# Kernel tuning notes

Hardware: AMD Instinct MI355X
Metric: run time of the kernel (lower is better)

The kernel has to match this reference:

```python
import jax, jax.numpy as jnp
import numpy as np

B, C, D = 4, 2048, 1024
DCONV, DMAMBA, K, DSTATE = 512, 512, 4, 16
FFN = 2560


def setup_inputs() -> dict:
    key = jax.random.key(0)
    ks = jax.random.split(key, 16)
    n = lambda k, shape, s=1.0: jax.random.normal(k, shape, jnp.float32) * s
    inv = lambda f: 1.0 / float(np.sqrt(f))
    return {
        "x": n(ks[0], (B, C, D)),
        "velocity": n(ks[1], (B, C, D), 0.1),
        "v_hat_chunk": n(ks[2], (B, C, D)),
        "delta_W": n(ks[3], (FFN, D), 0.01),
        "pre_norm_w": jnp.ones((D,), jnp.float32),
        "ffn_norm_w": jnp.ones((D,), jnp.float32),
        "conv_in_w": n(ks[4], (D, 2 * DCONV), inv(D)),
        "conv_kernel_w": n(ks[5], (K, 1, DCONV), inv(K)),
        "ssm_in_w": n(ks[6], (D, 2 * DMAMBA), inv(D)),
        "ssm_dt_w": n(ks[7], (D, DMAMBA), inv(D)),
        "ssm_dt_b": jnp.full((DMAMBA,), -4.0, jnp.float32),
        "ssm_A_log": jnp.tile(jnp.log(jnp.arange(1.0, DSTATE + 1, dtype=jnp.float32)), (DMAMBA, 1)),
        "ssm_B_w": n(ks[8], (D, DSTATE), inv(D)),
        "ssm_C_w": n(ks[9], (D, DSTATE), inv(D)),
        "ssm_D": jnp.ones((DMAMBA,), jnp.float32),
        "out_proj_w": n(ks[10], (D, D), inv(D)),
        "log_beta": jnp.array(0.0, jnp.float32),  # sigmoid -> beta=0.5
        "ffn_gate_up_w": n(ks[11], (D, 2 * FFN), inv(D)),
        "ffn_down_w": n(ks[12], (FFN, D), inv(FFN)),
        "ffn_target_w": n(ks[13], (D, FFN), inv(D)),
        "log_gamma": jnp.array(0.0, jnp.float32),
        "log_eta": jnp.array(-4.0, jnp.float32),
    }


def _rms(x, w, eps=1e-6):
    return x * jax.lax.rsqrt(jnp.mean(x * x, axis=-1, keepdims=True) + eps) * w


def _gated_conv(xn, w_in, kernel):
    # proj -> split gate/value, depthwise causal conv on value, silu-gate
    g, v = jnp.split(xn @ w_in, 2, axis=-1)  # (B,C,DCONV) each
    v = jax.lax.conv_general_dilated(
        v, kernel, window_strides=(1,), padding=[(K - 1, 0)],
        dimension_numbers=("NWC", "WIO", "NWC"), feature_group_count=DCONV)
    return jax.nn.silu(g) * v


def _ssm(xn, w_in, w_dt, dt_b, A_log, w_B, w_C, Dp):
    # Mamba-style selective SISO scan
    u, z = jnp.split(xn @ w_in, 2, axis=-1)          # (B,C,DMAMBA)
    dt = jax.nn.softplus(xn @ w_dt + dt_b)            # (B,C,DMAMBA)
    A = -jnp.exp(A_log)                               # (DMAMBA,DSTATE)
    Bs = xn @ w_B                                     # (B,C,DSTATE)
    Cs = xn @ w_C                                     # (B,C,DSTATE)
    dA = jnp.exp(dt[..., None] * A)                   # (B,C,DMAMBA,DSTATE)
    dBu = (dt * u)[..., None] * Bs[:, :, None, :]     # (B,C,DMAMBA,DSTATE)

    def step(h, inputs):
        dA_t, dBu_t, C_t = inputs
        h = dA_t * h + dBu_t                          # (B,DMAMBA,DSTATE)
        return h, jnp.einsum("bds,bs->bd", h, C_t)

    xs = (jnp.moveaxis(dA, 1, 0), jnp.moveaxis(dBu, 1, 0), jnp.moveaxis(Cs, 1, 0))
    _, ys = jax.lax.scan(step, jnp.zeros((B, DMAMBA, DSTATE), xn.dtype), xs)
    y = jnp.moveaxis(ys, 0, 1) + Dp * u               # (B,C,DMAMBA)
    return y * jax.nn.silu(z)


def reference(x, velocity, v_hat_chunk, delta_W, pre_norm_w, ffn_norm_w,
              conv_in_w, conv_kernel_w, ssm_in_w, ssm_dt_w, ssm_dt_b, ssm_A_log,
              ssm_B_w, ssm_C_w, ssm_D, out_proj_w, log_beta, ffn_gate_up_w,
              ffn_down_w, ffn_target_w, log_gamma, log_eta):
    xn = _rms(x, pre_norm_w)
    conv_out = _gated_conv(xn, conv_in_w, conv_kernel_w)
    ssm_out = _ssm(xn, ssm_in_w, ssm_dt_w, ssm_dt_b, ssm_A_log, ssm_B_w, ssm_C_w, ssm_D)
    mixed = jnp.concatenate([conv_out, ssm_out], axis=-1) @ out_proj_w
    # momentum residual
    velocity = jax.nn.sigmoid(log_beta) * velocity + mixed
    x = x + velocity
    # Living SwiGLU
    ffn_in = _rms(x, ffn_norm_w)
    gate, up = jnp.split(ffn_in @ ffn_gate_up_w, 2, axis=-1)
    z = jax.nn.silu(gate) * up                        # (B,C,FFN)
    out = z @ ffn_down_w + z @ delta_W                # fast-weight augmented down proj
    v_hat_proj = v_hat_chunk @ ffn_target_w           # (B,C,FFN)
    update = jnp.einsum("bcf,bcd->fd", v_hat_proj, ffn_in) / x.shape[0]
    new_delta_W = jax.nn.sigmoid(log_gamma) * delta_W + jax.nn.softplus(log_eta) * update
    x = x + out
    return (x, velocity, new_delta_W)
```

## Files before the change

kernel.cpp:

```cpp
#include <hip/hip_runtime.h>
#include <stdint.h>
#include <stddef.h>

#define B_ 4
#define C_ 2048
#define D_ 1024
#define FFN_ 2560
#define ROWS_ 8192

typedef unsigned short u16;
typedef short bf16x8 __attribute__((ext_vector_type(8)));
typedef float f32x4 __attribute__((ext_vector_type(4)));

__device__ __forceinline__ float bf2f(u16 x){ union { unsigned u; float f; } v; v.u = ((unsigned)x)<<16; return v.f; }
__device__ __forceinline__ u16 f2bf(float f){ union { float f; unsigned u; } v; v.f = f; unsigned r = v.u + 0x7fffu + ((v.u>>16)&1u); return (u16)(r>>16); }
__device__ __forceinline__ float sigm_(float x){ return 1.f/(1.f+__expf(-x)); }
__device__ __forceinline__ float silu_(float x){ return x/(1.f+__expf(-x)); }
__device__ __forceinline__ float softplus_(float x){ return (x>15.f)? x : log1pf(__expf(x)); }

__device__ __forceinline__ void async16(u16* lds_base, const u16* g){
  __builtin_amdgcn_global_load_lds((const __attribute__((address_space(1))) unsigned int*)g,
                                   (__attribute__((address_space(3))) unsigned int*)lds_base,
                                   16, 0, 0);
}

#define EPI_INPROJ 0
#define EPI_MOM    1
#define EPI_SWIGLU 2
#define EPI_TRANS  3
#define EPI_ATOMX  4
#define EPI_ATOMD  5

template<int EPI>
__global__ __launch_bounds__(256)
void gemm128(const u16* __restrict__ A, const u16* __restrict__ Bt,
             int M, int N, int K, int ksplit,
             float* __restrict__ f0, float* __restrict__ f1,
             const float* __restrict__ c0, const float* __restrict__ c1, const float* __restrict__ c2,
             u16* __restrict__ h0, u16* __restrict__ h1)
{
  __shared__ u16 smem[8192];
  u16* As = smem;
  u16* Bs = smem + 4096;
  const int tid  = threadIdx.x;
  const int wave = tid>>6, lane = tid&63;
  const int bm = blockIdx.y*128, bn = blockIdx.x*128;
  const int srow = wave*32 + (lane>>2);
  const int scol = (lane&3)*8;
  const u16* aG0 = A  + (size_t)(bm + srow)*K + scol;
  const u16* aG1 = aG0 + (size_t)16*K;
  const u16* bG0 = Bt + (size_t)(bn + srow)*K + scol;
  const u16* bG1 = bG0 + (size_t)16*K;
  u16* aL0 = As + (wave*2+0)*512;
  u16* aL1 = As + (wave*2+1)*512;
  u16* bL0 = Bs + (wave*2+0)*512;
  u16* bL1 = Bs + (wave*2+1)*512;
  const int wr = wave>>1, wc = wave&1;
  const int mrow = lane&15, quad = lane>>4;

  f32x4 acc[4][4];
  #pragma unroll
  for (int i=0;i<4;i++)
    #pragma unroll
    for (int j=0;j<4;j++) acc[i][j] = (f32x4){0.f,0.f,0.f,0.f};

  const int kbeg = blockIdx.z * ksplit;
  const int kend = kbeg + ksplit;
  for (int k0=kbeg; k0<kend; k0+=32){
    __syncthreads();
    async16(aL0, aG0 + k0);
    async16(aL1, aG1 + k0);
    async16(bL0, bG0 + k0);
    async16(bL1, bG1 + k0);
    __syncthreads();
    bf16x8 af[4], bfv[4];
    #pragma unroll
    for (int i=0;i<4;i++) af[i]  = *(const bf16x8*)(As + (wr*64+i*16+mrow)*32 + quad*8);
    #pragma unroll
    for (int j=0;j<4;j++) bfv[j] = *(const bf16x8*)(Bs + (wc*64+j*16+mrow)*32 + quad*8);
    #pragma unroll
    for (int i=0;i<4;i++)
      #pragma unroll
      for (int j=0;j<4;j++)
        acc[i][j] = __builtin_amdgcn_mfma_f32_16x16x32_bf16(af[i], bfv[j], acc[i][j], 0,0,0);
  }

  if constexpr (EPI == EPI_TRANS){
    __syncthreads();
    #pragma unroll
    for (int h=0; h<4; h++){
      const int hw = h>>1, j0 = (h&1)*2;
      if (wc == hw){
        #pragma unroll
        for (int i=0;i<4;i++){
          const int rbase = wr*64 + i*16 + quad*4;
          #pragma unroll
          for (int jj=0;jj<2;jj++){
            const int j = j0+jj;
            const int cl = jj*16 + mrow;
            f32x4 v = acc[i][j];
            #pragma unroll
            for (int t=0;t<4;t++) smem[cl*132 + rbase + t] = f2bf(v[t]);
          }
        }
      }
      __syncthreads();
      {
        const int cl2 = tid>>3, m0 = (tid&7)*16;
        const int col = bn + h*32 + cl2;
        const ushort4* s4 = (const ushort4*)(smem + cl2*132 + m0);
        ushort4* d4 = (ushort4*)(h0 + (size_t)col*M + bm + m0);
        #pragma unroll
        for (int q=0;q<4;q++) d4[q] = s4[q];
      }
      __syncthreads();
    }
  } else {
    #pragma unroll
    for (int i=0;i<4;i++){
      const int row0 = bm + wr*64 + i*16 + quad*4;
      if constexpr (EPI == EPI_SWIGLU){
        #pragma unroll
        for (int jp=0;jp<4;jp+=2){
          f32x4 g = acc[i][jp];
          f32x4 u = acc[i][jp+1];
          const int o = (((bn + wc*64 + jp*16)>>5)<<4) + mrow;
          #pragma unroll
          for (int t=0;t<4;t++) h0[(size_t)(row0+t)*2560 + o] = f2bf(silu_(g[t])*u[t]);
        }
      } else {
        #pragma unroll
        for (int j=0;j<4;j++){
          const int col = bn + wc*64 + j*16 + mrow;
          f32x4 v = acc[i][j];
          if constexpr (EPI == EPI_INPROJ){
            if (col < 1024){
              #pragma unroll
              for (int t=0;t<4;t++) h0[(size_t)(row0+t)*1024 + col] = f2bf(v[t]);
            } else if (col < 2048){
              #pragma unroll
              for (int t=0;t<4;t++) h1[(size_t)(row0+t)*1024 + (col-1024)] = f2bf(v[t]);
            } else if (col < 2560){
              const float b = c0[col-2048];
              #pragma unroll
              for (int t=0;t<4;t++) f0[(size_t)(row0+t)*512 + (col-2048)] = softplus_(v[t]+b);
            } else {
              const int cl = col - 2560;
              if (cl < 32){
                #pragma unroll
                for (int t=0;t<4;t++) f1[(size_t)(row0+t)*32 + cl] = v[t];
              }
            }
          } else if constexpr (EPI == EPI_MOM){
            const float beta = sigm_(c2[0]);
            #pragma unroll
            for (int t=0;t<4;t++){
              size_t idx = (size_t)(row0+t)*N + col;
              float vel = beta*c0[idx] + v[t];
              f0[idx] = vel;
              f1[idx] = c1[idx] + vel;
            }
          } else if constexpr (EPI == EPI_ATOMX){
            #pragma unroll
            for (int t=0;t<4;t++) atomicAdd(&f0[(size_t)(row0+t)*N + col], v[t]);
          } else if constexpr (EPI == EPI_ATOMD){
            const float e = softplus_(c2[0])*0.25f;
            #pragma unroll
            for (int t=0;t<4;t++) atomicAdd(&f0[(size_t)(row0+t)*N + col], e*v[t]);
          }
        }
      }
    }
  }
}

__global__ void prep_transposes(const float* __restrict__ conv_in_w, const float* __restrict__ ssm_in_w,
                                const float* __restrict__ ssm_dt_w, const float* __restrict__ out_proj_w,
                                const float* __restrict__ ffn_tgt_w, const float* __restrict__ gate_up_w,
                                u16* __restrict__ Wti, u16* __restrict__ out_proj_t,
                                u16* __restrict__ target_t, u16* __restrict__ gate_up_t)
{
  const int z = blockIdx.z;
  const float* W; u16* Wt; int N; bool gu = false;
  switch(z){
    case 0: W=conv_in_w;  Wt=Wti;                       N=1024; break;
    case 1: W=ssm_in_w;   Wt=Wti + (size_t)1024*1024;   N=1024; break;
    case 2: W=ssm_dt_w;   Wt=Wti + (size_t)2048*1024;   N=512;  break;
    case 3: W=out_proj_w; Wt=out_proj_t;                N=1024; break;
    case 4: W=ffn_tgt_w;  Wt=target_t;                  N=2560; break;
    default: W=gate_up_w; Wt=gate_up_t;                 N=5120; gu=true; break;
  }
  const int c0 = blockIdx.x*32, r0 = blockIdx.y*32;
  if (c0 >= N) return;
  __shared__ float tile[32][33];
  const int tx = threadIdx.x, ty = threadIdx.y;
  #pragma unroll
  for (int i=0;i<4;i++) tile[ty+8*i][tx] = W[(size_t)(r0+ty+8*i)*N + c0+tx];
  __syncthreads();
  #pragma unroll
  for (int i=0;i<4;i++){
    const int c = c0+ty+8*i;
    int n;
    if (gu){
      if (c < 2560) n = ((c>>4)<<5) | (c&15);
      else { int o = c-2560; n = ((o>>4)<<5) | 16 | (o&15); }
    } else n = c;
    Wt[(size_t)n*1024 + r0+tx] = f2bf(tile[tx][ty+8*i]);
  }
}

__global__ void weff_transpose(const float* __restrict__ Wa, const float* __restrict__ Wb, u16* __restrict__ Wt)
{
  __shared__ float tile[32][33];
  const int tx = threadIdx.x, ty = threadIdx.y;
  const int c0 = blockIdx.x*32, r0 = blockIdx.y*32;
  #pragma unroll
  for (int i=0;i<4;i++){
    size_t idx = (size_t)(r0+ty+8*i)*1024 + c0+tx;
    tile[ty+8*i][tx] = Wa[idx] + Wb[idx];
  }
  __syncthreads();
  #pragma unroll
  for (int i=0;i<4;i++) Wt[(size_t)(c0+ty+8*i)*2560 + r0+tx] = f2bf(tile[tx][ty+8*i]);
}

__global__ void transpose_bf16(const u16* __restrict__ in, u16* __restrict__ out, int R, int Cc)
{
  __shared__ u16 tile[32][33];
  const int tx = threadIdx.x, ty = threadIdx.y;
  const int c0 = blockIdx.x*32, r0 = blockIdx.y*32;
  #pragma unroll
  for (int i=0;i<4;i++) tile[ty+8*i][tx] = in[(size_t)(r0+ty+8*i)*Cc + c0+tx];
  __syncthreads();
  #pragma unroll
  for (int i=0;i<4;i++) out[(size_t)(c0+ty+8*i)*R + r0+tx] = tile[tx][ty+8*i];
}

__global__ void cvt_bf16x4(const float* __restrict__ in, u16* __restrict__ out, int n4)
{
  int i = blockIdx.x*256 + threadIdx.x;
  if (i < n4){
    float4 v = ((const float4*)in)[i];
    ushort4 p; p.x=f2bf(v.x); p.y=f2bf(v.y); p.z=f2bf(v.z); p.w=f2bf(v.w);
    ((ushort4*)out)[i] = p;
  }
}

__global__ void prep_small(const float* __restrict__ dW, const float* __restrict__ lg,
                           const float* __restrict__ Bw, const float* __restrict__ Cw,
                           const float* __restrict__ A_log,
                           float* __restrict__ out_delta, u16* __restrict__ bc_dst,
                           float* __restrict__ A_tab)
{
  const int blk = blockIdx.x, tid = threadIdx.x;
  if (blk < 2560){
    int i = blk*256 + tid;
    float g = sigm_(lg[0]);
    float4 v = ((const float4*)dW)[i];
    float4 r; r.x=g*v.x; r.y=g*v.y; r.z=g*v.z; r.w=g*v.w;
    ((float4*)out_delta)[i] = r;
  } else if (blk < 3072){
    int i = (blk-2560)*256 + tid;
    int r = i >> 10, k = i & 1023;
    float v = 0.f;
    if (r < 16) v = Bw[k*16 + r];
    else if (r < 32) v = Cw[k*16 + (r-16)];
    bc_dst[(size_t)r*1024 + k] = f2bf(v);
  } else {
    int i = (blk-3072)*256 + tid;
    if (i < 512*16) A_tab[i] = -__expf(A_log[i]);
  }
}

__global__ __launch_bounds__(256) void rmsnorm_k(const float* __restrict__ x, const float* __restrict__ w, u16* __restrict__ out)
{
  const int row = blockIdx.x, tid = threadIdx.x;
  float4 v = ((const float4*)(x + (size_t)row*1024))[tid];
  float s = v.x*v.x + v.y*v.y + v.z*v.z + v.w*v.w;
  #pragma unroll
  for (int o=32;o>0;o>>=1) s += __shfl_down(s, o);
  __shared__ float red[4];
  const int wave = tid>>6, lane = tid&63;
  if (lane==0) red[wave] = s;
  __syncthreads();
  float tot = red[0]+red[1]+red[2]+red[3];
  float sc = rsqrtf(tot*(1.f/1024.f) + 1e-6f);
  float4 wv = ((const float4*)w)[tid];
  ushort4 p; p.x=f2bf(v.x*sc*wv.x); p.y=f2bf(v.y*sc*wv.y); p.z=f2bf(v.z*sc*wv.z); p.w=f2bf(v.w*sc*wv.w);
  ((ushort4*)(out + (size_t)row*1024))[tid] = p;
}

__global__ __launch_bounds__(256) void conv_k(const u16* __restrict__ P1, const float* __restrict__ kw, u16* __restrict__ mixed)
{
  const int idx = blockIdx.x*256 + threadIdx.x;
  const int c = idx & 511;
  const int t = (idx>>9) & 2047;
  const int b = idx >> 20;
  const size_t rowb = (size_t)b*2048;
  float g = bf2f(P1[(rowb+t)*1024 + c]);
  float acc = 0.f;
  #pragma unroll
  for (int k=0;k<4;k++){
    int tt = t-3+k;
    if (tt>=0) acc += bf2f(P1[(rowb+tt)*1024 + 512 + c]) * kw[k*512+c];
  }
  mixed[(rowb+t)*1024 + c] = f2bf(silu_(g)*acc);
}

#define NCH_ 64
#define CHL_ 32
__global__ __launch_bounds__(256) void scan_p1(const float* __restrict__ dt, const u16* __restrict__ P2,
                                               const float* __restrict__ BCs, const float* __restrict__ A_tab,
                                               float* __restrict__ hend, float* __restrict__ aprod)
{
  const int d = blockIdx.x*256 + threadIdx.x;
  const int ch = blockIdx.y, b = blockIdx.z;
  float Ar[16], h[16], ap[16];
  #pragma unroll
  for (int s=0;s<16;s++){ Ar[s] = A_tab[d*16+s]; h[s]=0.f; ap[s]=1.f; }
  const int t0 = ch*CHL_;
  for (int t=0;t<CHL_;t++){
    size_t row = (size_t)b*2048 + t0 + t;
    float dtv = dt[row*512 + d];
    float u = bf2f(P2[row*1024 + d]);
    float du = dtv*u;
    const float* bs = BCs + row*32;
    #pragma unroll
    for (int s=0;s<16;s++){
      float dA = __expf(dtv*Ar[s]);
      h[s] = dA*h[s] + du*bs[s];
      ap[s] *= dA;
    }
  }
  size_t o = ((size_t)((b*512+d)*NCH_ + ch))*16;
  #pragma unroll
  for (int s=0;s<16;s++){ hend[o+s]=h[s]; aprod[o+s]=ap[s]; }
}

__global__ __launch_bounds__(256) void scan_p2(float* __restrict__ hend, const float* __restrict__ aprod)
{
  const int g = blockIdx.x*256 + threadIdx.x;
  const int s = g & 15, bd = g >> 4;
  float h = 0.f;
  for (int ch=0; ch<NCH_; ch++){
    size_t o = ((size_t)(bd*NCH_+ch))*16 + s;
    float he = hend[o], ap = aprod[o];
    hend[o] = h;
    h = ap*h + he;
  }
}

__global__ __launch_bounds__(256) void scan_p3(const float* __restrict__ dt, const u16* __restrict__ P2,
                                               const float* __restrict__ BCs, const float* __restrict__ A_tab,
                                               const float* __restrict__ hin, const float* __restrict__ Dp,
                                               u16* __restrict__ mixed)
{
  const int d = blockIdx.x*256 + threadIdx.x;
  const int ch = blockIdx.y, b = blockIdx.z;
  float Ar[16], h[16];
  size_t o = ((size_t)((b*512+d)*NCH_ + ch))*16;
  #pragma unroll
  for (int s=0;s<16;s++){ Ar[s] = A_tab[d*16+s]; h[s] = hin[o+s]; }
  const float Dd = Dp[d];
  const int t0 = ch*CHL_;
  for (int t=0;t<CHL_;t++){
    size_t row = (size_t)b*2048 + t0 + t;
    float dtv = dt[row*512 + d];
    float u = bf2f(P2[row*1024 + d]);
    float zv = bf2f(P2[row*1024 + 512 + d]);
    float du = dtv*u;
    const float* bs = BCs + row*32;
    const float* cs = bs + 16;
    float y = 0.f;
    #pragma unroll
    for (int s=0;s<16;s++){
      float dA = __expf(dtv*Ar[s]);
      h[s] = dA*h[s] + du*bs[s];
      y += h[s]*cs[s];
    }
    float outv = (y + Dd*u)*silu_(zv);
    mixed[row*1024 + 512 + d] = f2bf(outv);
  }
}

extern "C" void kernel_launch(void* const* d_in, const int* in_sizes, int n_in,
                              void* d_out, int out_size, void* d_ws, size_t ws_size,
                              hipStream_t stream)
{
  const float* x          = (const float*)d_in[0];
  const float* velocity   = (const float*)d_in[1];
  const float* v_hat      = (const float*)d_in[2];
  const float* delta_W    = (const float*)d_in[3];
  const float* pre_norm_w = (const float*)d_in[4];
  const float* ffn_norm_w = (const float*)d_in[5];
  const float* conv_in_w  = (const float*)d_in[6];
  const float* conv_kw    = (const float*)d_in[7];
  const float* ssm_in_w   = (const float*)d_in[8];
  const float* ssm_dt_w   = (const float*)d_in[9];
  const float* ssm_dt_b   = (const float*)d_in[10];
  const float* ssm_A_log  = (const float*)d_in[11];
  const float* ssm_B_w    = (const float*)d_in[12];
  const float* ssm_C_w    = (const float*)d_in[13];
  const float* ssm_D      = (const float*)d_in[14];
  const float* out_proj_w = (const float*)d_in[15];
  const float* log_beta   = (const float*)d_in[16];
  const float* gate_up_w  = (const float*)d_in[17];
  const float* ffn_down_w = (const float*)d_in[18];
  const float* ffn_tgt_w  = (const float*)d_in[19];
  const float* log_gamma  = (const float*)d_in[20];
  const float* log_eta    = (const float*)d_in[21];

  float* out_x     = (float*)d_out;
  float* out_vel   = out_x + (size_t)ROWS_*D_;
  float* out_delta = out_vel + (size_t)ROWS_*D_;

  char* wsp = (char*)d_ws;
  size_t off = 0;
  auto alloc = [&](size_t bytes)->char*{ char* p = wsp + off; off += (bytes + 255) & ~(size_t)255; return p; };

  u16* Wti        = (u16*)alloc((size_t)2688*1024*2);
  u16* out_proj_t = (u16*)alloc((size_t)1024*1024*2);
  u16* gate_up_t  = (u16*)alloc((size_t)5120*1024*2);
  u16* target_t   = (u16*)alloc((size_t)2560*1024*2);
  u16* weff_t     = (u16*)alloc((size_t)1024*2560*2);
  float* A_tab    = (float*)alloc((size_t)512*16*4);
  u16* xn         = (u16*)alloc((size_t)ROWS_*1024*2);
  u16* P1         = (u16*)alloc((size_t)ROWS_*1024*2);
  u16* P2         = (u16*)alloc((size_t)ROWS_*1024*2);
  float* dtbuf    = (float*)alloc((size_t)ROWS_*512*4);
  float* BCs      = (float*)alloc((size_t)ROWS_*32*4);
  float* hend     = (float*)alloc((size_t)4*512*NCH_*16*4);
  float* aprod    = (float*)alloc((size_t)4*512*NCH_*16*4);
  u16* mixed      = (u16*)alloc((size_t)ROWS_*1024*2);
  u16* ffn_in     = (u16*)alloc((size_t)ROWS_*1024*2);
  u16* zbuf       = (u16*)alloc((size_t)ROWS_*2560*2);
  u16* T1t        = (u16*)alloc((size_t)2560*ROWS_*2);
  u16* ffn_inT    = xn;
  u16* vhat_bf    = P1;

  dim3 tb(32,8);
  prep_transposes<<<dim3(160,32,6), tb, 0, stream>>>(conv_in_w, ssm_in_w, ssm_dt_w, out_proj_w,
      ffn_tgt_w, gate_up_w, Wti, out_proj_t, target_t, gate_up_t);
  weff_transpose<<<dim3(32,80), tb, 0, stream>>>(ffn_down_w, delta_W, weff_t);
  prep_small<<<3104, 256, 0, stream>>>(delta_W, log_gamma, ssm_B_w, ssm_C_w, ssm_A_log,
      out_delta, Wti + (size_t)2560*1024, A_tab);

  rmsnorm_k<<<ROWS_, 256, 0, stream>>>(x, pre_norm_w, xn);
  gemm128<EPI_INPROJ><<<dim3(21,64), 256, 0, stream>>>(xn, Wti, ROWS_,2688,1024,1024,
      dtbuf, BCs, ssm_dt_b, nullptr, nullptr, P1, P2);

  conv_k<<<16384, 256, 0, stream>>>(P1, conv_kw, mixed);
  scan_p1<<<dim3(2,NCH_,4), 256, 0, stream>>>(dtbuf, P2, BCs, A_tab, hend, aprod);
  scan_p2<<<128, 256, 0, stream>>>(hend, aprod);
  scan_p3<<<dim3(2,NCH_,4), 256, 0, stream>>>(dtbuf, P2, BCs, A_tab, hend, ssm_D, mixed);

  gemm128<EPI_MOM><<<dim3(8,64), 256, 0, stream>>>(mixed, out_proj_t, ROWS_,1024,1024,1024,
      out_vel, out_x, velocity, x, log_beta, nullptr, nullptr);

  rmsnorm_k<<<ROWS_, 256, 0, stream>>>(out_x, ffn_norm_w, ffn_in);
  transpose_bf16<<<dim3(32,256), tb, 0, stream>>>(ffn_in, ffn_inT, ROWS_, 1024);
  cvt_bf16x4<<<8192, 256, 0, stream>>>(v_hat, vhat_bf, ROWS_*1024/4);

  gemm128<EPI_SWIGLU><<<dim3(40,64), 256, 0, stream>>>(ffn_in, gate_up_t, ROWS_,5120,1024,1024,
      nullptr,nullptr,nullptr,nullptr,nullptr, zbuf, nullptr);
  gemm128<EPI_TRANS><<<dim3(20,64), 256, 0, stream>>>(vhat_bf, target_t, ROWS_,2560,1024,1024,
      nullptr,nullptr,nullptr,nullptr,nullptr, T1t, nullptr);

  gemm128<EPI_ATOMX><<<dim3(8,64,2), 256, 0, stream>>>(zbuf, weff_t, ROWS_,1024,2560,1280,
      out_x,nullptr,nullptr,nullptr,nullptr, nullptr,nullptr);

  gemm128<EPI_ATOMD><<<dim3(8,20,8), 256, 0, stream>>>(T1t, ffn_inT, 2560,1024,ROWS_,1024,
      out_delta,nullptr,nullptr,nullptr, log_eta, nullptr,nullptr);
}
```

Baseline: 882.3 us.

## Merge independent GEMMs into shared launches and widen K-tile with swizzled LDS

The v_hat target-projection GEMM now runs in the same launch as the input projection, selected by block index. The down-projection and delta-W update GEMMs also share one grid, with early returns for unused blocks. The GEMM K-step grows from 32 to 64, with an XOR-swizzled LDS layout to avoid bank conflicts, which doubles shared memory per block. The aim is fewer launches, fewer tail effects and fewer barriers per K, at the cost of occupancy and wasted blocks in the merged grid.

```diff
diff --git a/kernel.cpp b/kernel.cpp
--- a/kernel.cpp
+++ b/kernel.cpp
@@ -24,12 +24,10 @@
                                    16, 0, 0);
 }
 
-#define EPI_INPROJ 0
-#define EPI_MOM    1
-#define EPI_SWIGLU 2
-#define EPI_TRANS  3
-#define EPI_ATOMX  4
-#define EPI_ATOMD  5
+#define EPI_INTRANS   0
+#define EPI_MOM       1
+#define EPI_SWIGLU    2
+#define EPI_DOWNDELTA 3
 
 template<int EPI>
 __global__ __launch_bounds__(256)
@@ -37,26 +35,45 @@
              int M, int N, int K, int ksplit,
              float* __restrict__ f0, float* __restrict__ f1,
              const float* __restrict__ c0, const float* __restrict__ c1, const float* __restrict__ c2,
-             u16* __restrict__ h0, u16* __restrict__ h1)
-{
-  __shared__ u16 smem[8192];
+             u16* __restrict__ h0, u16* __restrict__ h1, u16* __restrict__ h2,
+             const u16* __restrict__ a2, const u16* __restrict__ b2)
+{
+  __shared__ u16 smem[16384];
   u16* As = smem;
-  u16* Bs = smem + 4096;
+  u16* Bs = smem + 8192;
   const int tid  = threadIdx.x;
   const int wave = tid>>6, lane = tid&63;
-  const int bm = blockIdx.y*128, bn = blockIdx.x*128;
-  const int srow = wave*32 + (lane>>2);
-  const int scol = (lane&3)*8;
-  const u16* aG0 = A  + (size_t)(bm + srow)*K + scol;
-  const u16* aG1 = aG0 + (size_t)16*K;
-  const u16* bG0 = Bt + (size_t)(bn + srow)*K + scol;
-  const u16* bG1 = bG0 + (size_t)16*K;
-  u16* aL0 = As + (wave*2+0)*512;
-  u16* aL1 = As + (wave*2+1)*512;
-  u16* bL0 = Bs + (wave*2+0)*512;
-  u16* bL1 = Bs + (wave*2+1)*512;
+
+  int bx = blockIdx.x;
+  bool alt = false;
+  if constexpr (EPI == EPI_INTRANS){
+    if (bx >= 21){ alt = true; bx -= 21; A = a2; Bt = b2; }
+  }
+  if constexpr (EPI == EPI_DOWNDELTA){
+    if (bx >= 8){
+      alt = true; bx -= 8;
+      if ((int)blockIdx.y >= 20) return;
+      A = a2; Bt = b2; K = 8192; ksplit = 2048;
+    } else {
+      if ((int)blockIdx.z >= 2) return;
+    }
+  }
+  const int bm = blockIdx.y*128, bn = bx*128;
+
+  const int lr8  = lane>>3;
+  const int kswz = ((lane&7) ^ lr8)*8;
+  const u16* aG[4]; const u16* bG[4]; u16* aL[4]; u16* bL[4];
+  #pragma unroll
+  for (int q=0;q<4;q++){
+    const int r = wave*32 + q*8 + lr8;
+    aG[q] = A  + (size_t)(bm + r)*K + kswz;
+    bG[q] = Bt + (size_t)(bn + r)*K + kswz;
+    aL[q] = As + (wave*32 + q*8)*64;
+    bL[q] = Bs + (wave*32 + q*8)*64;
+  }
   const int wr = wave>>1, wc = wave&1;
   const int mrow = lane&15, quad = lane>>4;
+  const int swz8 = (mrow&7);
 
   f32x4 acc[4][4];
   #pragma unroll
@@ -66,108 +83,135 @@
 
   const int kbeg = blockIdx.z * ksplit;
   const int kend = kbeg + ksplit;
-  for (int k0=kbeg; k0<kend; k0+=32){
+  for (int k0=kbeg; k0<kend; k0+=64){
     __syncthreads();
-    async16(aL0, aG0 + k0);
-    async16(aL1, aG1 + k0);
-    async16(bL0, bG0 + k0);
-    async16(bL1, bG1 + k0);
+    #pragma unroll
+    for (int q=0;q<4;q++) async16(aL[q], aG[q] + k0);
+    #pragma unroll
+    for (int q=0;q<4;q++) async16(bL[q], bG[q] + k0);
     __syncthreads();
-    bf16x8 af[4], bfv[4];
-    #pragma unroll
-    for (int i=0;i<4;i++) af[i]  = *(const bf16x8*)(As + (wr*64+i*16+mrow)*32 + quad*8);
-    #pragma unroll
-    for (int j=0;j<4;j++) bfv[j] = *(const bf16x8*)(Bs + (wc*64+j*16+mrow)*32 + quad*8);
-    #pragma unroll
-    for (int i=0;i<4;i++)
-      #pragma unroll
-      for (int j=0;j<4;j++)
-        acc[i][j] = __builtin_amdgcn_mfma_f32_16x16x32_bf16(af[i], bfv[j], acc[i][j], 0,0,0);
-  }
-
-  if constexpr (EPI == EPI_TRANS){
-    __syncthreads();
-    #pragma unroll
-    for (int h=0; h<4; h++){
-      const int hw = h>>1, j0 = (h&1)*2;
-      if (wc == hw){
+    #pragma unroll
+    for (int kk=0; kk<64; kk+=32){
+      bf16x8 af[4], bfv[4];
+      const int gq = (kk>>3) + quad;
+      const int pos = (gq ^ swz8)*8;
+      #pragma unroll
+      for (int i=0;i<4;i++) af[i]  = *(const bf16x8*)(As + (wr*64+i*16+mrow)*64 + pos);
+      #pragma unroll
+      for (int j=0;j<4;j++) bfv[j] = *(const bf16x8*)(Bs + (wc*64+j*16+mrow)*64 + pos);
+      #pragma unroll
+      for (int i=0;i<4;i++)
         #pragma unroll
-        for (int i=0;i<4;i++){
-          const int rbase = wr*64 + i*16 + quad*4;
+        for (int j=0;j<4;j++)
+          acc[i][j] = __builtin_amdgcn_mfma_f32_16x16x32_bf16(af[i], bfv[j], acc[i][j], 0,0,0);
+    }
+  }
+
+  if constexpr (EPI == EPI_INTRANS){
+    if (alt){
+      __syncthreads();
+      #pragma unroll
+      for (int h=0; h<4; h++){
+        const int hw = h>>1, j0 = (h&1)*2;
+        if (wc == hw){
           #pragma unroll
-          for (int jj=0;jj<2;jj++){
-            const int j = j0+jj;
-            const int cl = jj*16 + mrow;
-            f32x4 v = acc[i][j];
+          for (int i=0;i<4;i++){
+            const int rbase = wr*64 + i*16 + quad*4;
             #pragma unroll
-            for (int t=0;t<4;t++) smem[cl*132 + rbase + t] = f2bf(v[t]);
+            for (int jj=0;jj<2;jj++){
+              const int j = j0+jj;
+              const int cl = jj*16 + mrow;
+              f32x4 v = acc[i][j];
+              #pragma unroll
+              for (int t=0;t<4;t++) smem[cl*132 + rbase + t] = f2bf(v[t]);
+            }
           }
         }
+        __syncthreads();
+        {
+          const int cl2 = tid>>3, m0 = (tid&7)*16;
+          const int col = bn + h*32 + cl2;
+          const ushort4* s4 = (const ushort4*)(smem + cl2*132 + m0);
+          ushort4* d4 = (ushort4*)(h2 + (size_t)col*8192 + bm + m0);
+          #pragma unroll
+          for (int q=0;q<4;q++) d4[q] = s4[q];
+        }
+        __syncthreads();
       }
-      __syncthreads();
-      {
-        const int cl2 = tid>>3, m0 = (tid&7)*16;
-        const int col = bn + h*32 + cl2;
-        const ushort4* s4 = (const ushort4*)(smem + cl2*132 + m0);
-        ushort4* d4 = (ushort4*)(h0 + (size_t)col*M + bm + m0);
-        #pragma unroll
-        for (int q=0;q<4;q++) d4[q] = s4[q];
-      }
-      __syncthreads();
-    }
-  } else {
-    #pragma unroll
-    for (int i=0;i<4;i++){
-      const int row0 = bm + wr*64 + i*16 + quad*4;
-      if constexpr (EPI == EPI_SWIGLU){
-        #pragma unroll
-        for (int jp=0;jp<4;jp+=2){
-          f32x4 g = acc[i][jp];
-          f32x4 u = acc[i][jp+1];
-          const int o = (((bn + wc*64 + jp*16)>>5)<<4) + mrow;
-          #pragma unroll
-          for (int t=0;t<4;t++) h0[(size_t)(row0+t)*2560 + o] = f2bf(silu_(g[t])*u[t]);
-        }
-      } else {
+    } else {
+      #pragma unroll
+      for (int i=0;i<4;i++){
+        const int row0 = bm + wr*64 + i*16 + quad*4;
         #pragma unroll
         for (int j=0;j<4;j++){
           const int col = bn + wc*64 + j*16 + mrow;
           f32x4 v = acc[i][j];
-          if constexpr (EPI == EPI_INPROJ){
-            if (col < 1024){
+          if (col < 1024){
+            #pragma unroll
+            for (int t=0;t<4;t++) h0[(size_t)(row0+t)*1024 + col] = f2bf(v[t]);
+          } else if (col < 2048){
+            #pragma unroll
+            for (int t=0;t<4;t++) h1[(size_t)(row0+t)*1024 + (col-1024)] = f2bf(v[t]);
+          } else if (col < 2560){
+            const float b = c0[col-2048];
+            #pragma unroll
+            for (int t=0;t<4;t++) f0[(size_t)(row0+t)*512 + (col-2048)] = softplus_(v[t]+b);
+          } else {
+            const int cl = col - 2560;
+            if (cl < 32){
               #pragma unroll
-              for (int t=0;t<4;t++) h0[(size_t)(row0+t)*1024 + col] = f2bf(v[t]);
-            } else if (col < 2048){
-              #pragma unroll
-              for (int t=0;t<4;t++) h1[(size_t)(row0+t)*1024 + (col-1024)] = f2bf(v[t]);
-            } else if (col < 2560){
-              const float b = c0[col-2048];
-              #pragma unroll
-              for (int t=0;t<4;t++) f0[(size_t)(row0+t)*512 + (col-2048)] = softplus_(v[t]+b);
-            } else {
-              const int cl = col - 2560;
-              if (cl < 32){
-                #pragma unroll
-                for (int t=0;t<4;t++) f1[(size_t)(row0+t)*32 + cl] = v[t];
-              }
+              for (int t=0;t<4;t++) f1[(size_t)(row0+t)*32 + cl] = v[t];
             }
-          } else if constexpr (EPI == EPI_MOM){
-            const float beta = sigm_(c2[0]);
-            #pragma unroll
-            for (int t=0;t<4;t++){
-              size_t idx = (size_t)(row0+t)*N + col;
-              float vel = beta*c0[idx] + v[t];
-              f0[idx] = vel;
-              f1[idx] = c1[idx] + vel;
-            }
-          } else if constexpr (EPI == EPI_ATOMX){
-            #pragma unroll
-            for (int t=0;t<4;t++) atomicAdd(&f0[(size_t)(row0+t)*N + col], v[t]);
-          } else if constexpr (EPI == EPI_ATOMD){
-            const float e = softplus_(c2[0])*0.25f;
-            #pragma unroll
-            for (int t=0;t<4;t++) atomicAdd(&f0[(size_t)(row0+t)*N + col], e*v[t]);
           }
+        }
+      }
+    }
+  } else if constexpr (EPI == EPI_MOM){
+    const float beta = sigm_(c2[0]);
+    #pragma unroll
+    for (int i=0;i<4;i++){
+      const int row0 = bm + wr*64 + i*16 + quad*4;
+      #pragma unroll
+      for (int j=0;j<4;j++){
+        const int col = bn + wc*64 + j*16 + mrow;
+        f32x4 v = acc[i][j];
+        #pragma unroll
+        for (int t=0;t<4;t++){
+          size_t idx = (size_t)(row0+t)*1024 + col;
+          float vel = beta*c0[idx] + v[t];
+          f0[idx] = vel;
+          f1[idx] = c1[idx] + vel;
+        }
+      }
+    }
+  } else if constexpr (EPI == EPI_SWIGLU){
+    #pragma unroll
+    for (int i=0;i<4;i++){
+      const int row0 = bm + wr*64 + i*16 + quad*4;
+      #pragma unroll
+      for (int jp=0;jp<4;jp+=2){
+        f32x4 g = acc[i][jp];
+        f32x4 u = acc[i][jp+1];
+        const int o = (((bn + wc*64 + jp*16)>>5)<<4) + mrow;
+        #pragma unroll
+        for (int t=0;t<4;t++) h0[(size_t)(row0+t)*2560 + o] = f2bf(silu_(g[t])*u[t]);
+      }
+    }
+  } else if constexpr (EPI == EPI_DOWNDELTA){
+    #pragma unroll
+    for (int i=0;i<4;i++){
+      const int row0 = bm + wr*64 + i*16 + quad*4;
+      #pragma unroll
+      for (int j=0;j<4;j++){
+        const int col = bn + wc*64 + j*16 + mrow;
+        f32x4 v = acc[i][j];
+        if (!alt){
+          #pragma unroll
+          for (int t=0;t<4;t++) atomicAdd(&f0[(size_t)(row0+t)*1024 + col], v[t]);
+        } else {
+          const float e = softplus_(c2[0])*0.25f;
+          #pragma unroll
+          for (int t=0;t<4;t++) atomicAdd(&f1[(size_t)(row0+t)*1024 + col], e*v[t]);
         }
       }
     }
@@ -436,7 +480,7 @@
   u16* zbuf       = (u16*)alloc((size_t)ROWS_*2560*2);
   u16* T1t        = (u16*)alloc((size_t)2560*ROWS_*2);
   u16* ffn_inT    = xn;
-  u16* vhat_bf    = P1;
+  u16* vhat_bf    = mixed;
 
   dim3 tb(32,8);
   prep_transposes<<<dim3(160,32,6), tb, 0, stream>>>(conv_in_w, ssm_in_w, ssm_dt_w, out_proj_w,
@@ -444,10 +488,11 @@
   weff_transpose<<<dim3(32,80), tb, 0, stream>>>(ffn_down_w, delta_W, weff_t);
   prep_small<<<3104, 256, 0, stream>>>(delta_W, log_gamma, ssm_B_w, ssm_C_w, ssm_A_log,
       out_delta, Wti + (size_t)2560*1024, A_tab);
+  cvt_bf16x4<<<8192, 256, 0, stream>>>(v_hat, vhat_bf, ROWS_*1024/4);
 
   rmsnorm_k<<<ROWS_, 256, 0, stream>>>(x, pre_norm_w, xn);
-  gemm128<EPI_INPROJ><<<dim3(21,64), 256, 0, stream>>>(xn, Wti, ROWS_,2688,1024,1024,
-      dtbuf, BCs, ssm_dt_b, nullptr, nullptr, P1, P2);
+  gemm128<EPI_INTRANS><<<dim3(41,64), 256, 0, stream>>>(xn, Wti, ROWS_,2688,1024,1024,
+      dtbuf, BCs, ssm_dt_b, nullptr, nullptr, P1, P2, T1t, vhat_bf, target_t);
 
   conv_k<<<16384, 256, 0, stream>>>(P1, conv_kw, mixed);
   scan_p1<<<dim3(2,NCH_,4), 256, 0, stream>>>(dtbuf, P2, BCs, A_tab, hend, aprod);
@@ -455,20 +500,14 @@
   scan_p3<<<dim3(2,NCH_,4), 256, 0, stream>>>(dtbuf, P2, BCs, A_tab, hend, ssm_D, mixed);
 
   gemm128<EPI_MOM><<<dim3(8,64), 256, 0, stream>>>(mixed, out_proj_t, ROWS_,1024,1024,1024,
-      out_vel, out_x, velocity, x, log_beta, nullptr, nullptr);
+      out_vel, out_x, velocity, x, log_beta, nullptr, nullptr, nullptr, nullptr, nullptr);
 
   rmsnorm_k<<<ROWS_, 256, 0, stream>>>(out_x, ffn_norm_w, ffn_in);
   transpose_bf16<<<dim3(32,256), tb, 0, stream>>>(ffn_in, ffn_inT, ROWS_, 1024);
-  cvt_bf16x4<<<8192, 256, 0, stream>>>(v_hat, vhat_bf, ROWS_*1024/4);
 
   gemm128<EPI_SWIGLU><<<dim3(40,64), 256, 0, stream>>>(ffn_in, gate_up_t, ROWS_,5120,1024,1024,
-      nullptr,nullptr,nullptr,nullptr,nullptr, zbuf, nullptr);
-  gemm128<EPI_TRANS><<<dim3(20,64), 256, 0, stream>>>(vhat_bf, target_t, ROWS_,2560,1024,1024,
-      nullptr,nullptr,nullptr,nullptr,nullptr, T1t, nullptr);
-
-  gemm128<EPI_ATOMX><<<dim3(8,64,2), 256, 0, stream>>>(zbuf, weff_t, ROWS_,1024,2560,1280,
-      out_x,nullptr,nullptr,nullptr,nullptr, nullptr,nullptr);
-
-  gemm128<EPI_ATOMD><<<dim3(8,20,8), 256, 0, stream>>>(T1t, ffn_inT, 2560,1024,ROWS_,1024,
-      out_delta,nullptr,nullptr,nullptr, log_eta, nullptr,nullptr);
-}
+      nullptr,nullptr,nullptr,nullptr,nullptr, zbuf, nullptr, nullptr, nullptr, nullptr);
+
+  gemm128<EPI_DOWNDELTA><<<dim3(16,64,4), 256, 0, stream>>>(zbuf, weff_t, ROWS_,1024,2560,1280,
+      out_x, out_delta, nullptr, nullptr, log_eta, nullptr, nullptr, nullptr, T1t, ffn_inT);
+}
```

After: 877.5 us. Within noise of the previous version (-0.5%).
